# Performance work log

Hardware: AMD Instinct MI355X
Metric: run time of the kernel (lower is better)

The kernel has to match this reference:

```python
import jax, jax.numpy as jnp
import numpy as np

V, D, U, L, B, T = 32000, 256, 512, 2, 16, 128


def _lstm_stack(x, mask, params):
    """Stacked LSTM over time-major x [T,B,D] with mask [T,B].
    Keras LSTMCell gate order i,f,g,o; masked steps carry previous h,c."""
    nb = x.shape[1]
    init = tuple((jnp.zeros((nb, U), x.dtype), jnp.zeros((nb, U), x.dtype)) for _ in params)

    def step(carry, inp):
        xt, mt = inp
        m = mt[:, None]
        new = []
        h_in = xt
        for (W, Uw, b), (h, c) in zip(params, carry):
            z = h_in @ W + h @ Uw + b          # [B, 4U]
            i, f, g, o = jnp.split(z, 4, axis=-1)
            c_new = jax.nn.sigmoid(f) * c + jax.nn.sigmoid(i) * jnp.tanh(g)
            h_new = jax.nn.sigmoid(o) * jnp.tanh(c_new)
            h_new = jnp.where(m, h_new, h)
            c_new = jnp.where(m, c_new, c)
            new.append((h_new, c_new))
            h_in = h_new
        return tuple(new), h_in

    _, ys = jax.lax.scan(step, init, (x, mask))
    return ys  # [T, B, U]


def setup_inputs() -> dict:
    key = jax.random.key(0)
    ks = jax.random.split(key, 16)
    s = 0.05
    seqs = jax.random.randint(ks[0], (B, T), 0, V)
    embed = jax.random.normal(ks[1], (V, D), dtype=jnp.float32) * 0.01

    def lstm_p(k, din):
        k1, k2 = jax.random.split(k)
        return (jax.random.normal(k1, (din, 4 * U), dtype=jnp.float32) * s,
                jax.random.normal(k2, (U, 4 * U), dtype=jnp.float32) * s,
                jnp.zeros((4 * U,), dtype=jnp.float32))

    fW0, fU0, fb0 = lstm_p(ks[2], D)
    fW1, fU1, fb1 = lstm_p(ks[3], U)
    bW0, bU0, bb0 = lstm_p(ks[4], D)
    bW1, bU1, bb1 = lstm_p(ks[5], U)
    Wp = jax.random.normal(ks[6], (2 * U, V), dtype=jnp.float32) * s
    bp = jnp.zeros((V,), dtype=jnp.float32)
    return {"seqs": seqs, "embed": embed,
            "fW0": fW0, "fU0": fU0, "fb0": fb0, "fW1": fW1, "fU1": fU1, "fb1": fb1,
            "bW0": bW0, "bU0": bU0, "bb0": bb0, "bW1": bW1, "bU1": bU1, "bb1": bb1,
            "Wp": Wp, "bp": bp}


def reference(seqs, embed, fW0, fU0, fb0, fW1, fU1, fb1,
              bW0, bU0, bb0, bW1, bU1, bb1, Wp, bp):
    emb = embed[seqs]                      # [B, T, D]
    mask = seqs != 0                       # mask_zero=True
    # forward LSTM over tokens 0..T-2
    fx = jnp.swapaxes(emb[:, :-1], 0, 1)   # [T-1, B, D]
    fm = jnp.swapaxes(mask[:, :-1], 0, 1)
    f = jnp.swapaxes(_lstm_stack(fx, fm, [(fW0, fU0, fb0), (fW1, fU1, fb1)]), 0, 1)  # [B,T-1,U]
    # backward LSTM (go_backwards): process tokens 1..T-1 reversed in time
    bx = jnp.swapaxes(emb[:, 1:][:, ::-1], 0, 1)
    bm = jnp.swapaxes(mask[:, 1:][:, ::-1], 0, 1)
    b = jnp.swapaxes(_lstm_stack(bx, bm, [(bW0, bU0, bb0), (bW1, bU1, bb1)]), 0, 1)  # reversed-time order
    b_rev = b[:, ::-1]                     # tf.reverse(b, axis=[1]) -> natural order
    o = jnp.concatenate([f[:, :-1], b_rev[:, 1:]], axis=-1)  # [B, T-2, 2U]
    word_logits = o @ Wp + bp              # [B, T-2, V]
    return word_logits
```

## Files before the change

kernel.cpp:

```cpp
#include <hip/hip_runtime.h>

#define VOCAB 32000
#define DIM   256
#define UN    512
#define TT    128
#define T1    126
#define NG    2048
#define NBLK  256

typedef __attribute__((ext_vector_type(8))) __bf16 bf16x8;
typedef __attribute__((ext_vector_type(4))) float  f32x4;

__device__ __forceinline__ unsigned short f2bf(float f) {
  union { float f; unsigned u; } v; v.f = f;
  unsigned r = (v.u + 0x7fffu + ((v.u >> 16) & 1u)) >> 16;
  return (unsigned short)r;
}
__device__ __forceinline__ float f4_get(const float4& v, int j) {
  return j == 0 ? v.x : j == 1 ? v.y : j == 2 ? v.z : v.w;
}
__device__ __forceinline__ void async16(const void* g, void* l) {
  __builtin_amdgcn_global_load_lds((const __attribute__((address_space(1))) void*)g,
                                   (__attribute__((address_space(3))) void*)l, 16, 0, 0);
}

__global__ __launch_bounds__(256) void k_gather(const int* __restrict__ seqs,
                                                const float* __restrict__ embed,
                                                float* __restrict__ emb) {
  int idx = blockIdx.x * 256 + threadIdx.x;
  int d4 = idx & 63, bt = idx >> 6;
  int tok = seqs[bt];
  ((float4*)emb)[idx] = ((const float4*)embed)[(size_t)tok * 64 + d4];
}

__global__ __launch_bounds__(256, 2) void k_zin(const float* __restrict__ emb,
    const float* __restrict__ fW0, const float* __restrict__ fb0,
    const float* __restrict__ bW0, const float* __restrict__ bb0,
    float* __restrict__ Z0) {
  __shared__ __align__(16) float xs[16 * 260];
  int bi = blockIdx.x;
  int jh  = bi & 1;
  int t   = (bi >> 1) % T1;
  int dir = (bi >> 1) / T1;
  int tim = dir ? (TT - 1) - t : t;
  const float* W    = dir ? bW0 : fW0;
  const float* bias = dir ? bb0 : fb0;
  int tid = threadIdx.x;
  #pragma unroll
  for (int i = 0; i < 4; ++i) {
    int fidx = i * 256 + tid;
    int b = fidx >> 6, k4 = fidx & 63;
    float4 v = ((const float4*)emb)[(size_t)(b * TT + tim) * 64 + k4];
    *(float4*)&xs[b * 260 + k4 * 4] = v;
  }
  __syncthreads();
  int j0 = jh * 1024 + tid;
  float acc[4][16];
  #pragma unroll
  for (int q = 0; q < 4; ++q) {
    float bv = bias[j0 + q * 256];
    #pragma unroll
    for (int b = 0; b < 16; ++b) acc[q][b] = bv;
  }
  #pragma unroll 2
  for (int k = 0; k < DIM; k += 4) {
    float4 xv[16];
    #pragma unroll
    for (int b = 0; b < 16; ++b) xv[b] = *(const float4*)&xs[b * 260 + k];
    #pragma unroll
    for (int kk = 0; kk < 4; ++kk) {
      float w[4];
      #pragma unroll
      for (int q = 0; q < 4; ++q) w[q] = W[(size_t)(k + kk) * NG + j0 + q * 256];
      #pragma unroll
      for (int q = 0; q < 4; ++q)
        #pragma unroll
        for (int b = 0; b < 16; ++b)
          acc[q][b] += f4_get(xv[b], kk) * w[q];
    }
  }
  float* out = Z0 + ((size_t)(dir * T1 + t) * 16) * NG;
  #pragma unroll
  for (int q = 0; q < 4; ++q)
    #pragma unroll
    for (int b = 0; b < 16; ++b)
      out[(size_t)b * NG + j0 + q * 256] = acc[q][b];
}

__global__ __launch_bounds__(256) void k_cast_wp(const float* __restrict__ Wp,
                                                 unsigned short* __restrict__ Bt) {
  __shared__ float tile[32][33];
  int bi = blockIdx.x;
  int kt = bi & 31, nt = bi >> 5;
  int k0 = kt * 32, n0 = nt * 32;
  int tid = threadIdx.x;
  int nl = tid & 31, kl = tid >> 5;
  #pragma unroll
  for (int i = 0; i < 4; ++i) {
    int k = kl + i * 8;
    tile[k][nl] = Wp[(size_t)(k0 + k) * VOCAB + n0 + nl];
  }
  __syncthreads();
  int kl2 = tid & 31, nl2 = tid >> 5;
  #pragma unroll
  for (int i = 0; i < 4; ++i) {
    int n = nl2 + i * 8;
    Bt[(size_t)(n0 + n) * 1024 + k0 + kl2] = f2bf(tile[kl2][n]);
  }
}

__global__ __launch_bounds__(256) void k_padA(unsigned short* __restrict__ A) {
  int idx = blockIdx.x * 256 + threadIdx.x;
  ((uint4*)(A + (size_t)2016 * 1024))[idx] = make_uint4(0u, 0u, 0u, 0u);
}


__device__ __forceinline__ void waitcnt_group(const int* g, int target) {
  if (threadIdx.x == 0) {
    for (;;) {
      int s = 0;
      #pragma unroll
      for (int i = 0; i < 8; ++i)
        s += __hip_atomic_load((const int*)(g + i * 32), __ATOMIC_RELAXED,
                               __HIP_MEMORY_SCOPE_AGENT);
      if (s >= target) break;
      __builtin_amdgcn_s_sleep(1);
    }
  }
  __syncthreads();
}

__device__ __forceinline__ void waitcnt_group2(const int* g1, int t1,
                                               const int* g2, int t2) {
  if (threadIdx.x == 0) {
    for (;;) {
      int s1 = 0, s2 = 0;
      #pragma unroll
      for (int i = 0; i < 8; ++i) {
        s1 += __hip_atomic_load((const int*)(g1 + i * 32), __ATOMIC_RELAXED,
                                __HIP_MEMORY_SCOPE_AGENT);
        s2 += __hip_atomic_load((const int*)(g2 + i * 32), __ATOMIC_RELAXED,
                                __HIP_MEMORY_SCOPE_AGENT);
      }
      if (s1 >= t1 && s2 >= t2) break;
      __builtin_amdgcn_s_sleep(1);
    }
  }
  __syncthreads();
}

__device__ __forceinline__ void signal_group(int* sub) {
  __builtin_amdgcn_s_waitcnt(0);
  __syncthreads();
  if (threadIdx.x == 0)
    __hip_atomic_fetch_add(sub, 1, __ATOMIC_RELAXED, __HIP_MEMORY_SCOPE_AGENT);
}

__device__ __forceinline__ void stage1(float* xs, const float* __restrict__ src) {
  const int tid = threadIdx.x;
  #pragma unroll
  for (int i = 0; i < 8; ++i) {
    const int fidx = i * 256 + tid;
    const int b = fidx >> 7, k = (fidx & 127) * 4;
    const float4 v = src ? *(const float4*)&src[(size_t)b * 512 + k]
                         : make_float4(0.f, 0.f, 0.f, 0.f);
    *(float4*)&xs[b * 640 + (k >> 4) * 20 + (k & 15)] = v;
  }
}

__device__ __forceinline__ void stage2(float* xsA, const float* __restrict__ srcA,
                                       float* xsB, const float* __restrict__ srcB) {
  const int tid = threadIdx.x;
  float4 va[8], vb[8];
  #pragma unroll
  for (int i = 0; i < 8; ++i) {
    const int fidx = i * 256 + tid;
    const int b = fidx >> 7, k = (fidx & 127) * 4;
    va[i] = *(const float4*)&srcA[(size_t)b * 512 + k];
    vb[i] = srcB ? *(const float4*)&srcB[(size_t)b * 512 + k]
                 : make_float4(0.f, 0.f, 0.f, 0.f);
  }
  #pragma unroll
  for (int i = 0; i < 8; ++i) {
    const int fidx = i * 256 + tid;
    const int b = fidx >> 7, k = (fidx & 127) * 4;
    *(float4*)&xsA[b * 640 + (k >> 4) * 20 + (k & 15)] = va[i];
    *(float4*)&xsB[b * 640 + (k >> 4) * 20 + (k & 15)] = vb[i];
  }
}

__device__ __forceinline__ void phase_acc(const float* xs, const float (&u)[4][16],
                                          float (&acc)[4][16], int kp) {
  const float* xb = xs + kp * 20;
  #pragma unroll
  for (int kk4 = 0; kk4 < 4; ++kk4) {
    float4 xv[16];
    #pragma unroll
    for (int b = 0; b < 16; ++b) xv[b] = *(const float4*)&xb[b * 640 + kk4 * 4];
    #pragma unroll
    for (int j = 0; j < 4; ++j)
      #pragma unroll
      for (int g = 0; g < 4; ++g) {
        float uv = u[g][kk4 * 4 + j];
        #pragma unroll
        for (int b = 0; b < 16; ++b) acc[g][b] += f4_get(xv[b], j) * uv;
      }
  }
}

template <int LAYER>
__device__ void recur_path(const int* __restrict__ seqs,
                           const float* __restrict__ Z0,
                           const float* __restrict__ P1,
                           const float* __restrict__ P2,
                           const float* __restrict__ b1,
                           float* __restrict__ H0,
                           float* __restrict__ h1,
                           unsigned short* __restrict__ A,
                           int* cnt_own, int* sub_own, int* cnt_l0,
                           float* xsA, float* xsB, float* red,
                           int dir, int u0)
{
  const int tid = threadIdx.x;
  const int kp = tid >> 3;
  const int unit = u0 + (tid & 7);
  float u1r[4][16], u2r[4][16];
  #pragma unroll
  for (int g = 0; g < 4; ++g)
    #pragma unroll
    for (int kk = 0; kk < 16; ++kk) {
      const int col = g * UN + unit;
      u1r[g][kk] = P1[(size_t)(kp * 16 + kk) * NG + col];
      if (LAYER) u2r[g][kk] = P2[(size_t)(kp * 16 + kk) * NG + col];
    }
  const int cu = tid & 7, cb = tid >> 3;
  const int un = u0 + cu;
  float b1r[4] = {0.f, 0.f, 0.f, 0.f};
  if (LAYER && tid < 128) {
    #pragma unroll
    for (int g = 0; g < 4; ++g) b1r[g] = b1[g * UN + un];
  }
  float hst = 0.f, cstate = 0.f;

  for (int t = 0; t < 126; ++t) {
    float zp[4] = {0.f, 0.f, 0.f, 0.f};
    bool m = false;
    if (tid < 128) {
      const int tim = dir ? (TT - 1) - t : t;
      m = seqs[cb * TT + tim] != 0;
      if (LAYER == 0) {
        const float* zr = Z0 + (((size_t)dir * T1 + t) * 16 + cb) * NG;
        #pragma unroll
        for (int g = 0; g < 4; ++g) zp[g] = zr[g * UN + un];
      }
    }
    if (LAYER == 0) {
      if (t == 0) {
        stage1(xsA, nullptr);
      } else {
        waitcnt_group(cnt_own, 64 * t);
        stage1(xsA, H0 + ((size_t)(dir * T1 + (t - 1)) * 16) * UN);
      }
    } else {
      const float* srcA = H0 + ((size_t)(dir * T1 + t) * 16) * UN;
      if (t == 0) {
        waitcnt_group(cnt_l0, 64);
        stage2(xsA, srcA, xsB, nullptr);
      } else {
        waitcnt_group2(cnt_l0, 64 * (t + 1), cnt_own, 64 * t);
        stage2(xsA, srcA, xsB, h1 + ((size_t)((t - 1) * 2 + dir) * 16) * UN);
      }
    }
    __syncthreads();

    float acc[4][16];
    #pragma unroll
    for (int g = 0; g < 4; ++g)
      #pragma unroll
      for (int b = 0; b < 16; ++b) acc[g][b] = 0.f;
    phase_acc(xsA, u1r, acc, kp);
    if (LAYER) phase_acc(xsB, u2r, acc, kp);

    #pragma unroll
    for (int g = 0; g < 4; ++g)
      #pragma unroll
      for (int b = 0; b < 16; ++b) {
        float v = acc[g][b];
        v += __shfl_xor(v, 8);
        v += __shfl_xor(v, 16);
        v += __shfl_xor(v, 32);
        acc[g][b] = v;
      }
    const int lane = tid & 63, wv = tid >> 6;
    if (lane < 8) {
      #pragma unroll
      for (int g = 0; g < 4; ++g)
        #pragma unroll
        for (int b = 0; b < 16; ++b)
          red[((wv * 8 + lane) * 4 + g) * 17 + b] = acc[g][b];
    }
    __syncthreads();

    if (tid < 128) {
      float z[4];
      #pragma unroll
      for (int g = 0; g < 4; ++g) {
        float v = red[(cu * 4 + g) * 17 + cb];
        #pragma unroll
        for (int w = 1; w < 4; ++w) v += red[((w * 8 + cu) * 4 + g) * 17 + cb];
        z[g] = v + (LAYER ? b1r[g] : zp[g]);
      }
      const float si = 1.f / (1.f + expf(-z[0]));
      const float sf = 1.f / (1.f + expf(-z[1]));
      const float tg = tanhf(z[2]);
      const float so = 1.f / (1.f + expf(-z[3]));
      const float cn = sf * cstate + si * tg;
      const float hn = so * tanhf(cn);
      const float hsel = m ? hn : hst;
      const float csel = m ? cn : cstate;
      cstate = csel; hst = hsel;
      if (LAYER == 0) {
        __hip_atomic_store(&H0[(((size_t)dir * T1 + t) * 16 + cb) * UN + un],
                           hsel, __ATOMIC_RELAXED, __HIP_MEMORY_SCOPE_AGENT);
      } else {
        __hip_atomic_store(&h1[(((size_t)t * 2 + dir) * 16 + cb) * UN + un],
                           hsel, __ATOMIC_RELAXED, __HIP_MEMORY_SCOPE_AGENT);
        const int row = dir ? (125 - t) : t;
        A[((size_t)cb * T1 + row) * 1024 + dir * UN + un] = f2bf(hsel);
      }
    }
    signal_group(sub_own);
  }
}

__global__ __launch_bounds__(256, 1) void k_recur(
    const int* __restrict__ seqs, const float* __restrict__ Z0,
    const float* __restrict__ fU0, const float* __restrict__ bU0,
    const float* __restrict__ fW1, const float* __restrict__ fU1, const float* __restrict__ fb1,
    const float* __restrict__ bW1, const float* __restrict__ bU1, const float* __restrict__ bb1,
    float* __restrict__ H0, float* __restrict__ h1, unsigned short* __restrict__ A,
    int* __restrict__ bar)
{
  __shared__ __align__(16) float xs[2][16 * 640];
  __shared__ float red[32 * 4 * 17];
  const int bi = blockIdx.x;
  const int dir = (bi >> 6) & 1;
  const int u0 = (bi & 63) * 8;
  const int gid = bi >> 6;
  int* cnt_own = bar + gid * 256;
  int* sub_own = cnt_own + (bi & 7) * 32;
  int* cnt_l0  = bar + dir * 256;
  if ((bi >> 7) == 0)
    recur_path<0>(seqs, Z0, dir ? bU0 : fU0, nullptr, nullptr,
                  H0, h1, A, cnt_own, sub_own, cnt_l0, xs[0], xs[1], red, dir, u0);
  else
    recur_path<1>(seqs, Z0, dir ? bW1 : fW1, dir ? bU1 : fU1, dir ? bb1 : fb1,
                  H0, h1, A, cnt_own, sub_own, cnt_l0, xs[0], xs[1], red, dir, u0);
}

__global__ __launch_bounds__(256, 2) void k_proj(
    const unsigned short* __restrict__ Abf, const unsigned short* __restrict__ Bt,
    const float* __restrict__ bp, float* __restrict__ out)
{
  __shared__ unsigned short As[128 * 32];
  __shared__ unsigned short Bs[128 * 32];
  int bi = blockIdx.x;
  int mt = bi & 15, nt = bi >> 4;
  int m0 = mt * 128, n0 = nt * 128;
  int tid = threadIdx.x;
  int wv = tid >> 6, lane = tid & 63;
  int wm = wv & 1, wn = wv >> 1;
  f32x4 acc[4][4] = {};
  for (int kt = 0; kt < 32; ++kt) {
    int r0 = wv * 32;
    #pragma unroll
    for (int i = 0; i < 2; ++i) {
      int row = r0 + i * 16 + (lane >> 2);
      const unsigned short* ga = Abf + (size_t)(m0 + row) * 1024 + kt * 32 + (lane & 3) * 8;
      async16(ga, As + (r0 + i * 16) * 32);
      const unsigned short* gb = Bt + (size_t)(n0 + row) * 1024 + kt * 32 + (lane & 3) * 8;
      async16(gb, Bs + (r0 + i * 16) * 32);
    }
    __syncthreads();
    bf16x8 af[4], bf[4];
    #pragma unroll
    for (int i = 0; i < 4; ++i) {
      int m = wm * 64 + i * 16 + (lane & 15);
      af[i] = *(const bf16x8*)&As[m * 32 + (lane >> 4) * 8];
      int n = wn * 64 + i * 16 + (lane & 15);
      bf[i] = *(const bf16x8*)&Bs[n * 32 + (lane >> 4) * 8];
    }
    #pragma unroll
    for (int i = 0; i < 4; ++i)
      #pragma unroll
      for (int j = 0; j < 4; ++j)
        acc[i][j] = __builtin_amdgcn_mfma_f32_16x16x32_bf16(af[i], bf[j], acc[i][j], 0, 0, 0);
    __syncthreads();
  }
  #pragma unroll
  for (int j = 0; j < 4; ++j) {
    int col = n0 + wn * 64 + j * 16 + (lane & 15);
    float bv = bp[col];
    #pragma unroll
    for (int i = 0; i < 4; ++i) {
      int rbase = m0 + wm * 64 + i * 16 + (lane >> 4) * 4;
      #pragma unroll
      for (int r = 0; r < 4; ++r) {
        int row = rbase + r;
        if (row < 2016) out[(size_t)row * VOCAB + col] = acc[i][j][r] + bv;
      }
    }
  }
}

extern "C" void kernel_launch(void* const* d_in, const int* in_sizes, int n_in,
                              void* d_out, int out_size, void* d_ws, size_t ws_size,
                              hipStream_t stream)
{
  const int*   seqs  = (const int*)  d_in[0];
  const float* embed = (const float*)d_in[1];
  const float* fW0 = (const float*)d_in[2];
  const float* fU0 = (const float*)d_in[3];
  const float* fb0 = (const float*)d_in[4];
  const float* fW1 = (const float*)d_in[5];
  const float* fU1 = (const float*)d_in[6];
  const float* fb1 = (const float*)d_in[7];
  const float* bW0 = (const float*)d_in[8];
  const float* bU0 = (const float*)d_in[9];
  const float* bb0 = (const float*)d_in[10];
  const float* bW1 = (const float*)d_in[11];
  const float* bU1 = (const float*)d_in[12];
  const float* bb1 = (const float*)d_in[13];
  const float* Wp  = (const float*)d_in[14];
  const float* bp  = (const float*)d_in[15];
  float* out = (float*)d_out;

  char* ws = (char*)d_ws;
  float* emb   = (float*)(ws);
  float* Z0    = (float*)(ws + 2097152);
  float* H0    = (float*)(ws + 35127296);
  float* h1    = (float*)(ws + 43384832);
  unsigned short* A  = (unsigned short*)(ws + 51642368);
  unsigned short* Bt = (unsigned short*)(ws + 55836672);
  int* bar = (int*)(ws + 1048576);

  hipLaunchKernelGGL(k_gather, dim3(512), dim3(256), 0, stream, seqs, embed, emb);
  hipLaunchKernelGGL(k_zin, dim3(504), dim3(256), 0, stream, emb, fW0, fb0, bW0, bb0, Z0);
  hipLaunchKernelGGL(k_cast_wp, dim3(32000), dim3(256), 0, stream, Wp, Bt);
  hipLaunchKernelGGL(k_padA, dim3(16), dim3(256), 0, stream, A);
  hipMemsetAsync(bar, 0, 4096, stream);

  void* rargs[] = {(void*)&seqs, (void*)&Z0, (void*)&fU0, (void*)&bU0,
                   (void*)&fW1, (void*)&fU1, (void*)&fb1,
                   (void*)&bW1, (void*)&bU1, (void*)&bb1,
                   (void*)&H0, (void*)&h1, (void*)&A, (void*)&bar};
  hipError_t ce = hipLaunchCooperativeKernel((void*)k_recur, dim3(NBLK), dim3(256),
                                             rargs, 0, stream);
  if (ce != hipSuccess) {
    (void)hipGetLastError();
    hipLaunchKernelGGL(k_recur, dim3(NBLK), dim3(256), 0, stream,
                       seqs, Z0, fU0, bU0, fW1, fU1, fb1, bW1, bU1, bb1,
                       H0, h1, A, bar);
  }

  hipLaunchKernelGGL(k_proj, dim3(4000), dim3(256), 0, stream, A, Bt, bp, out);
}
```

Baseline: 2.306 ms.

## Replace summed-counter polling with hierarchical epoch barrier and split layer-1 waits

```diff
diff --git a/kernel.cpp b/kernel.cpp
--- a/kernel.cpp
+++ b/kernel.cpp
@@ -115,77 +115,49 @@
 }
 
 
-__device__ __forceinline__ void waitcnt_group(const int* g, int target) {
+__device__ __forceinline__ void wait_epoch(const int* ep, int target) {
   if (threadIdx.x == 0) {
-    for (;;) {
-      int s = 0;
-      #pragma unroll
-      for (int i = 0; i < 8; ++i)
-        s += __hip_atomic_load((const int*)(g + i * 32), __ATOMIC_RELAXED,
-                               __HIP_MEMORY_SCOPE_AGENT);
-      if (s >= target) break;
-      __builtin_amdgcn_s_sleep(1);
-    }
+    while (__hip_atomic_load(ep, __ATOMIC_RELAXED, __HIP_MEMORY_SCOPE_AGENT) < target)
+      __builtin_amdgcn_s_sleep(2);
   }
   __syncthreads();
 }
 
-__device__ __forceinline__ void waitcnt_group2(const int* g1, int t1,
-                                               const int* g2, int t2) {
-  if (threadIdx.x == 0) {
-    for (;;) {
-      int s1 = 0, s2 = 0;
-      #pragma unroll
-      for (int i = 0; i < 8; ++i) {
-        s1 += __hip_atomic_load((const int*)(g1 + i * 32), __ATOMIC_RELAXED,
-                                __HIP_MEMORY_SCOPE_AGENT);
-        s2 += __hip_atomic_load((const int*)(g2 + i * 32), __ATOMIC_RELAXED,
-                                __HIP_MEMORY_SCOPE_AGENT);
-      }
-      if (s1 >= t1 && s2 >= t2) break;
-      __builtin_amdgcn_s_sleep(1);
-    }
-  }
-  __syncthreads();
-}
-
-__device__ __forceinline__ void signal_group(int* sub) {
+__device__ __forceinline__ void signal_step(int* grp, int sub_idx, int s) {
   __builtin_amdgcn_s_waitcnt(0);
   __syncthreads();
-  if (threadIdx.x == 0)
-    __hip_atomic_fetch_add(sub, 1, __ATOMIC_RELAXED, __HIP_MEMORY_SCOPE_AGENT);
-}
-
-__device__ __forceinline__ void stage1(float* xs, const float* __restrict__ src) {
+  if (threadIdx.x == 0) {
+    int old = __hip_atomic_fetch_add(grp + sub_idx * 32, 1,
+                                     __ATOMIC_RELAXED, __HIP_MEMORY_SCOPE_AGENT);
+    if (old == 8 * (s + 1) - 1) {
+      int mold = __hip_atomic_fetch_add(grp + 256, 1,
+                                        __ATOMIC_RELAXED, __HIP_MEMORY_SCOPE_AGENT);
+      if (mold == 8 * (s + 1) - 1) {
+        #pragma unroll
+        for (int i = 0; i < 8; ++i)
+          __hip_atomic_store(grp + 512 + i * 32, s + 1,
+                             __ATOMIC_RELAXED, __HIP_MEMORY_SCOPE_AGENT);
+      }
+    }
+  }
+}
+
+__device__ __forceinline__ void ldstage_regs(float4 (&v)[8], const float* __restrict__ src) {
   const int tid = threadIdx.x;
   #pragma unroll
   for (int i = 0; i < 8; ++i) {
     const int fidx = i * 256 + tid;
     const int b = fidx >> 7, k = (fidx & 127) * 4;
-    const float4 v = src ? *(const float4*)&src[(size_t)b * 512 + k]
-                         : make_float4(0.f, 0.f, 0.f, 0.f);
-    *(float4*)&xs[b * 640 + (k >> 4) * 20 + (k & 15)] = v;
-  }
-}
-
-__device__ __forceinline__ void stage2(float* xsA, const float* __restrict__ srcA,
-                                       float* xsB, const float* __restrict__ srcB) {
+    v[i] = *(const float4*)&src[(size_t)b * 512 + k];
+  }
+}
+__device__ __forceinline__ void ldswrite(float* xs, const float4 (&v)[8]) {
   const int tid = threadIdx.x;
-  float4 va[8], vb[8];
   #pragma unroll
   for (int i = 0; i < 8; ++i) {
     const int fidx = i * 256 + tid;
     const int b = fidx >> 7, k = (fidx & 127) * 4;
-    va[i] = *(const float4*)&srcA[(size_t)b * 512 + k];
-    vb[i] = srcB ? *(const float4*)&srcB[(size_t)b * 512 + k]
-                 : make_float4(0.f, 0.f, 0.f, 0.f);
-  }
-  #pragma unroll
-  for (int i = 0; i < 8; ++i) {
-    const int fidx = i * 256 + tid;
-    const int b = fidx >> 7, k = (fidx & 127) * 4;
-    *(float4*)&xsA[b * 640 + (k >> 4) * 20 + (k & 15)] = va[i];
-    *(float4*)&xsB[b * 640 + (k >> 4) * 20 + (k & 15)] = vb[i];
+    *(float4*)&xs[b * 640 + (k >> 4) * 20 + (k & 15)] = v[i];
   }
 }
 
@@ -217,7 +189,8 @@
                            float* __restrict__ H0,
                            float* __restrict__ h1,
                            unsigned short* __restrict__ A,
-                           int* cnt_own, int* sub_own, int* cnt_l0,
+                           int* grp_own, int sub_idx,
+                           const int* ep_own, const int* ep_l0,
                            float* xsA, float* xsB, float* red,
                            int dir, int u0)
 {
@@ -255,21 +228,28 @@
       }
     }
     if (LAYER == 0) {
+      float4 va[8];
       if (t == 0) {
-        stage1(xsA, nullptr);
+        #pragma unroll
+        for (int i = 0; i < 8; ++i) va[i] = make_float4(0.f, 0.f, 0.f, 0.f);
       } else {
-        waitcnt_group(cnt_own, 64 * t);
-        stage1(xsA, H0 + ((size_t)(dir * T1 + (t - 1)) * 16) * UN);
-      }
+        wait_epoch(ep_own, t);
+        ldstage_regs(va, H0 + ((size_t)(dir * T1 + (t - 1)) * 16) * UN);
+      }
+      ldswrite(xsA, va);
     } else {
-      const float* srcA = H0 + ((size_t)(dir * T1 + t) * 16) * UN;
-      if (t == 0) {
-        waitcnt_group(cnt_l0, 64);
-        stage2(xsA, srcA, xsB, nullptr);
+      float4 va[8], vb[8];
+      if (t >= 1) {
+        wait_epoch(ep_own, t);
+        ldstage_regs(vb, h1 + ((size_t)((t - 1) * 2 + dir) * 16) * UN);
       } else {
-        waitcnt_group2(cnt_l0, 64 * (t + 1), cnt_own, 64 * t);
-        stage2(xsA, srcA, xsB, h1 + ((size_t)((t - 1) * 2 + dir) * 16) * UN);
-      }
+        #pragma unroll
+        for (int i = 0; i < 8; ++i) vb[i] = make_float4(0.f, 0.f, 0.f, 0.f);
+      }
+      wait_epoch(ep_l0, t + 1);
+      ldstage_regs(va, H0 + ((size_t)(dir * T1 + t) * 16) * UN);
+      ldswrite(xsB, vb);
+      ldswrite(xsA, va);
     }
     __syncthreads();
 
@@ -329,7 +309,7 @@
         A[((size_t)cb * T1 + row) * 1024 + dir * UN + un] = f2bf(hsel);
       }
     }
-    signal_group(sub_own);
+    signal_step(grp_own, sub_idx, t);
   }
 }
 
@@ -347,15 +327,17 @@
   const int dir = (bi >> 6) & 1;
   const int u0 = (bi & 63) * 8;
   const int gid = bi >> 6;
-  int* cnt_own = bar + gid * 256;
-  int* sub_own = cnt_own + (bi & 7) * 32;
-  int* cnt_l0  = bar + dir * 256;
+  int* grp_own = bar + gid * 1024;
+  const int* ep_own = grp_own + 512 + (bi & 7) * 32;
+  const int* ep_l0  = bar + dir * 1024 + 512 + (bi & 7) * 32;
   if ((bi >> 7) == 0)
     recur_path<0>(seqs, Z0, dir ? bU0 : fU0, nullptr, nullptr,
-                  H0, h1, A, cnt_own, sub_own, cnt_l0, xs[0], xs[1], red, dir, u0);
+                  H0, h1, A, grp_own, bi & 7, ep_own, ep_l0,
+                  xs[0], xs[1], red, dir, u0);
   else
     recur_path<1>(seqs, Z0, dir ? bW1 : fW1, dir ? bU1 : fU1, dir ? bb1 : fb1,
-                  H0, h1, A, cnt_own, sub_own, cnt_l0, xs[0], xs[1], red, dir, u0);
+                  H0, h1, A, grp_own, bi & 7, ep_own, ep_l0,
+                  xs[0], xs[1], red, dir, u0);
 }
 
 __global__ __launch_bounds__(256, 2) void k_proj(
@@ -448,7 +430,7 @@
   hipLaunchKernelGGL(k_zin, dim3(504), dim3(256), 0, stream, emb, fW0, fb0, bW0, bb0, Z0);
   hipLaunchKernelGGL(k_cast_wp, dim3(32000), dim3(256), 0, stream, Wp, Bt);
   hipLaunchKernelGGL(k_padA, dim3(16), dim3(256), 0, stream, A);
-  hipMemsetAsync(bar, 0, 4096, stream);
+  hipMemsetAsync(bar, 0, 16384, stream);
 
   void* rargs[] = {(void*)&seqs, (void*)&Z0, (void*)&fU0, (void*)&bU0,
                    (void*)&fW1, (void*)&fU1, (void*)&fb1,
```

Result: faster. 2.088 ms (-9.5%).
